# Kernel tuning notes

Measured on AMD Instinct MI355X. Metric: run time of the kernel, lower is better.

## Reference

```python
import jax, jax.numpy as jnp
import numpy as np

M = 8        # number of input features
NMF = 4      # membership functions per feature
R = NMF ** M # 65536 rules
N = 1024     # batch size


def setup_inputs() -> dict:
    key = jax.random.key(0)
    k1, k2, k3, k4, k5 = jax.random.split(key, 5)
    x = jax.random.normal(k1, (N, M), dtype=jnp.float32)
    # Antecedent parameters: torch.rand -> uniform [0,1)
    center = jax.random.uniform(k2, (M, NMF), dtype=jnp.float32)
    sigma = jax.random.uniform(k3, (M, NMF), dtype=jnp.float32)
    # Consequent linear layer, init_Consequent uses uniform [0,1)
    W = jax.random.uniform(k4, (R, M), dtype=jnp.float32)
    b = jax.random.uniform(k5, (R,), dtype=jnp.float32)
    return {"x": x, "center": center, "sigma": sigma, "W": W, "b": b}


def reference(x, center, sigma, W, b):
    # droprule=False (deterministic reference; the torch drop_rule is random Bernoulli masking)
    n = x.shape[0]
    # Gaussian membership, faithful to torch: exp(-(x - c)^2 / 2 * sigma^2)
    # mg: [N, M, NMF]
    mg = jnp.exp(-((x[:, :, None] - center[None, :, :]) ** 2) * 0.5 * (sigma[None, :, :] ** 2))
    # Combinatorial rule product via mixed-radix broadcasting:
    # fg[n, r] = prod_m mg[n, m, digit_m(r)], feature 0 most significant.
    fg = mg[:, 0, :]  # [N, NMF]
    for m in range(1, M):
        fg = (fg[:, :, None] * mg[:, m, None, :]).reshape(n, -1)
    # fg: [N, R]
    fg_bar = fg / jnp.sum(fg, axis=1, keepdims=True)
    rule_out = x @ W.T + b  # [N, R]
    return jnp.sum(fg_bar * rule_out, axis=1)  # [N]
```

## Files before the change

kernel.cpp:

```cpp
#include <hip/hip_runtime.h>

typedef __attribute__((ext_vector_type(8))) short short8;
typedef __attribute__((ext_vector_type(4))) float f32x4;

#define KB 16
#define ROWP 16

__device__ __forceinline__ ushort f2bf_rne(float f) {
    union { float f; unsigned u; } v; v.f = f;
    unsigned r = v.u + 0x7FFF + ((v.u >> 16) & 1);
    return (ushort)(r >> 16);
}

__global__ __launch_bounds__(256) void fz_main(
    const float* __restrict__ x, const float* __restrict__ center,
    const float* __restrict__ sigma, const float* __restrict__ W,
    const float* __restrict__ b, float* __restrict__ S , int N)
{
    __shared__ float  mgs[16][32];
    __shared__ ushort plf[8][64][8];
    __shared__ float  phs[16][KB];
    __shared__ float  red[4][16][9];

    const int t = threadIdx.x;
    const int tile = blockIdx.x >> 4;
    const int kb = blockIdx.x & (KB - 1);

    #pragma unroll
    for (int v = 0; v < 2; ++v) {
        int id = t + v * 256;
        int s = id >> 5, i = id & 31, m = i >> 2;
        float xv = x[(size_t)(tile * 16 + s) * 8 + m];
        float d = xv - center[i];
        float sg = sigma[i];
        mgs[s][i] = __expf(-d * d * 0.5f * sg * sg);
    }
    __syncthreads();
    {
        short8 o0, o1;
        #pragma unroll
        for (int u = 0; u < 16; ++u) {
            int e = t * 16 + u;
            int ls = e >> 9, lane = (e >> 3) & 63, j = e & 7;
            int s = lane & 15;
            int lo = ls * 32 + (lane >> 4) * 8 + j;
            float pl = mgs[s][16 + (lo >> 6)] * mgs[s][20 + ((lo >> 4) & 3)]
                     * mgs[s][24 + ((lo >> 2) & 3)] * mgs[s][28 + (lo & 3)];
            if (u < 8) o0[u] = (short)f2bf_rne(pl);
            else       o1[u - 8] = (short)f2bf_rne(pl);
        }
        short8* dst = reinterpret_cast<short8*>(((ushort*)plf) + t * 16);
        dst[0] = o0; dst[1] = o1;
    }
    {
        int s = t >> 4, hl = t & 15;
        int hi = kb * KB + hl;
        phs[s][hl] = mgs[s][hi >> 6] * mgs[s][4 + ((hi >> 4) & 3)]
                   * mgs[s][8 + ((hi >> 2) & 3)] * mgs[s][12 + (hi & 3)];
    }
    __syncthreads();

    const int wv = t >> 6, lane = t & 63;
    const int c = lane & 15, kb4 = lane >> 4;
    short8 A[8];
    #pragma unroll
    for (int ls = 0; ls < 8; ++ls)
        A[ls] = *reinterpret_cast<const short8*>(&plf[ls][lane][0]);

    const float* src = (c < 8) ? (W + c) : b;
    const int stride = (c < 8) ? 8 : 1;
    const bool live = (c <= 8);

    f32x4 master = {0.f, 0.f, 0.f, 0.f};
    const int hi_base = kb * KB + wv * 4;
    #pragma unroll
    for (int hil = 0; hil < 4; ++hil) {
        const int hi = hi_base + hil;
        f32x4 d = {0.f, 0.f, 0.f, 0.f};
        #pragma unroll
        for (int ls = 0; ls < 8; ++ls) {
            const int rbase = hi * 256 + ls * 32 + kb4 * 8;
            unsigned u[8];
            #pragma unroll
            for (int j = 0; j < 8; ++j) {
                union { float f; unsigned v; } q;
                q.f = src[(size_t)(rbase + j) * stride];
                u[j] = q.v;
            }
            unsigned Bp[4];
            #pragma unroll
            for (int j2 = 0; j2 < 4; ++j2) {
                unsigned lo16 = (u[2 * j2] + 0x8000u) >> 16;
                unsigned hi16 = (u[2 * j2 + 1] + 0x8000u) & 0xFFFF0000u;
                Bp[j2] = live ? (hi16 | lo16) : 0u;
            }
            short8 B = *reinterpret_cast<short8*>(&Bp[0]);
            d = __builtin_amdgcn_mfma_f32_16x16x32_bf16(A[ls], B, d, 0, 0, 0);
        }
        const int srow = kb4 * 4;
        #pragma unroll
        for (int r = 0; r < 4; ++r)
            master[r] += phs[srow + r][wv * 4 + hil] * d[r];
    }

    if (c < 9) {
        #pragma unroll
        for (int r = 0; r < 4; ++r)
            red[wv][kb4 * 4 + r][c] = master[r];
    }
    __syncthreads();
    if (t < 144) {
        int s = t / 9, cc = t % 9;
        float v = red[0][s][cc] + red[1][s][cc] + red[2][s][cc] + red[3][s][cc];
        S[((size_t)kb * N + tile * 16 + s) * ROWP + cc] = v;
    }
}

__global__ __launch_bounds__(256) void fz_final(
    const float* __restrict__ x, const float* __restrict__ center,
    const float* __restrict__ sigma, const float* __restrict__ S,
    float* __restrict__ out, int N)
{
    int n = blockIdx.x * 256 + threadIdx.x;
    if (n >= N) return;
    float xv[8];
    #pragma unroll
    for (int m = 0; m < 8; ++m) xv[m] = x[(size_t)n * 8 + m];
    float denom = 1.f;
    #pragma unroll
    for (int m = 0; m < 8; ++m) {
        float ssum = 0.f;
        #pragma unroll
        for (int j = 0; j < 4; ++j) {
            float d = xv[m] - center[m * 4 + j];
            float sg = sigma[m * 4 + j];
            ssum += expf(-d * d * 0.5f * sg * sg);
        }
        denom *= ssum;
    }
    float sc[9];
    #pragma unroll
    for (int cc = 0; cc < 9; ++cc) sc[cc] = 0.f;
    #pragma unroll
    for (int ch = 0; ch < KB; ++ch) {
        const float* p = S + ((size_t)ch * N + n) * ROWP;
        const float4 a  = *reinterpret_cast<const float4*>(p);
        const float4 bq = *reinterpret_cast<const float4*>(p + 4);
        sc[0] += a.x;  sc[1] += a.y;  sc[2] += a.z;  sc[3] += a.w;
        sc[4] += bq.x; sc[5] += bq.y; sc[6] += bq.z; sc[7] += bq.w;
        sc[8] += p[8];
    }
    float num = sc[8];
    #pragma unroll
    for (int m = 0; m < 8; ++m) num += xv[m] * sc[m];
    out[n] = num / denom;
}

extern "C" void kernel_launch(void* const* d_in, const int* in_sizes, int n_in,
                              void* d_out, int out_size, void* d_ws, size_t ws_size,
                              hipStream_t stream)
{
    const float* x      = (const float*)d_in[0];
    const float* center = (const float*)d_in[1];
    const float* sigma  = (const float*)d_in[2];
    const float* W      = (const float*)d_in[3];
    const float* b      = (const float*)d_in[4];
    float* out = (float*)d_out;
    const int N = in_sizes[0] / 8;

    float* S = (float*)d_ws;

    fz_main<<<(N / 16) * KB, 256, 0, stream>>>(x, center, sigma, W, b, S, N);
    fz_final<<<(N + 255) / 256, 256, 0, stream>>>(x, center, sigma, S, out, N);
}
```

Before: 85.33 us.

## Software-pipeline W loads, factor rule-product precompute, and shrink final-kernel blocks

The main loop is flattened into 32 steps with double-buffered register prefetch of the next W/b slice, so global loads for one step overlap the MFMA of the previous one. The low-feature rule product is factored through a small shared table of pairwise products with padded shared arrays, and rounding switches to a simpler round-half-up bf16 conversion. The final kernel uses 64-thread blocks to spread its work over more CUs and uses the fast __expf. The prefetch buffers raise register pressure, and the rounding change alters numerics slightly.

Measured after the change: 76.67 us. -10.1%, faster.

```diff
diff --git a/kernel.cpp b/kernel.cpp
--- a/kernel.cpp
+++ b/kernel.cpp
@@ -6,20 +6,15 @@
 #define KB 16
 #define ROWP 16
 
-__device__ __forceinline__ ushort f2bf_rne(float f) {
-    union { float f; unsigned u; } v; v.f = f;
-    unsigned r = v.u + 0x7FFF + ((v.u >> 16) & 1);
-    return (ushort)(r >> 16);
-}
-
 __global__ __launch_bounds__(256) void fz_main(
     const float* __restrict__ x, const float* __restrict__ center,
     const float* __restrict__ sigma, const float* __restrict__ W,
     const float* __restrict__ b, float* __restrict__ S , int N)
 {
-    __shared__ float  mgs[16][32];
+    __shared__ float  mgs[16][33];
+    __shared__ float  pr[16][20];
     __shared__ ushort plf[8][64][8];
-    __shared__ float  phs[16][KB];
+    __shared__ float  phs[16][17];
     __shared__ float  red[4][16][9];
 
     const int t = threadIdx.x;
@@ -37,26 +32,37 @@
     }
     __syncthreads();
     {
-        short8 o0, o1;
+        int s = t >> 4, a = t & 15;
+        pr[s][a] = mgs[s][24 + (a >> 2)] * mgs[s][28 + (a & 3)];
+        int hi = kb * KB + a;
+        phs[s][a] = mgs[s][hi >> 6] * mgs[s][4 + ((hi >> 4) & 3)]
+                  * mgs[s][8 + ((hi >> 2) & 3)] * mgs[s][12 + (hi & 3)];
+    }
+    __syncthreads();
+    {
+        const int ls = t >> 5;
         #pragma unroll
-        for (int u = 0; u < 16; ++u) {
-            int e = t * 16 + u;
-            int ls = e >> 9, lane = (e >> 3) & 63, j = e & 7;
-            int s = lane & 15;
-            int lo = ls * 32 + (lane >> 4) * 8 + j;
-            float pl = mgs[s][16 + (lo >> 6)] * mgs[s][20 + ((lo >> 4) & 3)]
-                     * mgs[s][24 + ((lo >> 2) & 3)] * mgs[s][28 + (lo & 3)];
-            if (u < 8) o0[u] = (short)f2bf_rne(pl);
-            else       o1[u - 8] = (short)f2bf_rne(pl);
+        for (int oct = 0; oct < 2; ++oct) {
+            const int lane_e = (2 * t + oct) & 63;
+            const int s = lane_e & 15;
+            const int hi3 = lane_e >> 4;
+            const int L0 = ls * 32 + hi3 * 8;
+            const float pqv = mgs[s][16 + (L0 >> 6)] * mgs[s][20 + ((L0 >> 4) & 3)];
+            const int b7 = L0 & 8;
+            const float4 r0 = *reinterpret_cast<const float4*>(&pr[s][b7]);
+            const float4 r1 = *reinterpret_cast<const float4*>(&pr[s][b7 + 4]);
+            float pv[8] = { pqv * r0.x, pqv * r0.y, pqv * r0.z, pqv * r0.w,
+                            pqv * r1.x, pqv * r1.y, pqv * r1.z, pqv * r1.w };
+            unsigned Pk[4];
+            #pragma unroll
+            for (int j2 = 0; j2 < 4; ++j2) {
+                union { float f; unsigned u; } a0, a1;
+                a0.f = pv[2 * j2]; a1.f = pv[2 * j2 + 1];
+                Pk[j2] = ((a0.u + 0x8000u) >> 16) | ((a1.u + 0x8000u) & 0xFFFF0000u);
+            }
+            *reinterpret_cast<short8*>(&plf[ls][lane_e][0]) =
+                *reinterpret_cast<short8*>(&Pk[0]);
         }
-        short8* dst = reinterpret_cast<short8*>(((ushort*)plf) + t * 16);
-        dst[0] = o0; dst[1] = o1;
-    }
-    {
-        int s = t >> 4, hl = t & 15;
-        int hi = kb * KB + hl;
-        phs[s][hl] = mgs[s][hi >> 6] * mgs[s][4 + ((hi >> 4) & 3)]
-                   * mgs[s][8 + ((hi >> 2) & 3)] * mgs[s][12 + (hi & 3)];
     }
     __syncthreads();
 
@@ -69,38 +75,43 @@
 
     const float* src = (c < 8) ? (W + c) : b;
     const int stride = (c < 8) ? 8 : 1;
-    const bool live = (c <= 8);
+    const unsigned lmask = (c <= 8) ? 0xFFFFFFFFu : 0u;
+
+    const int hi_base = kb * KB + wv * 4;
+    const float* p = src + (size_t)(hi_base * 256 + kb4 * 8) * stride;
+    const ptrdiff_t s32 = (ptrdiff_t)32 * stride;
+
+    float buf[2][8];
+    #pragma unroll
+    for (int j = 0; j < 8; ++j) buf[0][j] = p[j * stride];
 
     f32x4 master = {0.f, 0.f, 0.f, 0.f};
-    const int hi_base = kb * KB + wv * 4;
+    f32x4 d = {0.f, 0.f, 0.f, 0.f};
     #pragma unroll
-    for (int hil = 0; hil < 4; ++hil) {
-        const int hi = hi_base + hil;
-        f32x4 d = {0.f, 0.f, 0.f, 0.f};
+    for (int step = 0; step < 32; ++step) {
+        const float* pn = p + s32;
+        if (step < 31) {
+            #pragma unroll
+            for (int j = 0; j < 8; ++j) buf[(step + 1) & 1][j] = pn[j * stride];
+        }
+        const float* cu = buf[step & 1];
+        unsigned Bp[4];
         #pragma unroll
-        for (int ls = 0; ls < 8; ++ls) {
-            const int rbase = hi * 256 + ls * 32 + kb4 * 8;
-            unsigned u[8];
+        for (int j2 = 0; j2 < 4; ++j2) {
+            union { float f; unsigned u; } a0, a1;
+            a0.f = cu[2 * j2]; a1.f = cu[2 * j2 + 1];
+            Bp[j2] = (((a0.u + 0x8000u) >> 16) | ((a1.u + 0x8000u) & 0xFFFF0000u)) & lmask;
+        }
+        short8 B = *reinterpret_cast<short8*>(&Bp[0]);
+        d = __builtin_amdgcn_mfma_f32_16x16x32_bf16(A[step & 7], B, d, 0, 0, 0);
+        if ((step & 7) == 7) {
+            const int hil = step >> 3;
             #pragma unroll
-            for (int j = 0; j < 8; ++j) {
-                union { float f; unsigned v; } q;
-                q.f = src[(size_t)(rbase + j) * stride];
-                u[j] = q.v;
-            }
-            unsigned Bp[4];
-            #pragma unroll
-            for (int j2 = 0; j2 < 4; ++j2) {
-                unsigned lo16 = (u[2 * j2] + 0x8000u) >> 16;
-                unsigned hi16 = (u[2 * j2 + 1] + 0x8000u) & 0xFFFF0000u;
-                Bp[j2] = live ? (hi16 | lo16) : 0u;
-            }
-            short8 B = *reinterpret_cast<short8*>(&Bp[0]);
-            d = __builtin_amdgcn_mfma_f32_16x16x32_bf16(A[ls], B, d, 0, 0, 0);
+            for (int r = 0; r < 4; ++r)
+                master[r] += phs[kb4 * 4 + r][wv * 4 + hil] * d[r];
+            d = (f32x4){0.f, 0.f, 0.f, 0.f};
         }
-        const int srow = kb4 * 4;
-        #pragma unroll
-        for (int r = 0; r < 4; ++r)
-            master[r] += phs[srow + r][wv * 4 + hil] * d[r];
+        p = pn;
     }
 
     if (c < 9) {
@@ -116,12 +127,12 @@
     }
 }
 
-__global__ __launch_bounds__(256) void fz_final(
+__global__ __launch_bounds__(64) void fz_final(
     const float* __restrict__ x, const float* __restrict__ center,
     const float* __restrict__ sigma, const float* __restrict__ S,
     float* __restrict__ out, int N)
 {
-    int n = blockIdx.x * 256 + threadIdx.x;
+    int n = blockIdx.x * 64 + threadIdx.x;
     if (n >= N) return;
     float xv[8];
     #pragma unroll
@@ -132,9 +143,9 @@
         float ssum = 0.f;
         #pragma unroll
         for (int j = 0; j < 4; ++j) {
-            float d = xv[m] - center[m * 4 + j];
+            float dd = xv[m] - center[m * 4 + j];
             float sg = sigma[m * 4 + j];
-            ssum += expf(-d * d * 0.5f * sg * sg);
+            ssum += __expf(-dd * dd * 0.5f * sg * sg);
         }
         denom *= ssum;
     }
@@ -171,5 +182,5 @@
     float* S = (float*)d_ws;
 
     fz_main<<<(N / 16) * KB, 256, 0, stream>>>(x, center, sigma, W, b, S, N);
-    fz_final<<<(N + 255) / 256, 256, 0, stream>>>(x, center, sigma, S, out, N);
+    fz_final<<<(N + 63) / 64, 64, 0, stream>>>(x, center, sigma, S, out, N);
 }
```
